# Kernel tuning notes

Measured on AMD Instinct MI355X. Metric: run time of the kernel, lower is better.

The kernel has to match this reference:

```python
import jax, jax.numpy as jnp
import numpy as np

N = 100000   # nodes
C = 128      # in_channels
K = 32       # n_super_nodes
B = 64       # graphs (num segments)


def setup_inputs() -> dict:
    key = jax.random.key(0)
    k_x, k_b, k_w1, k_b1, k_w2, k_b2 = jax.random.split(key, 6)
    x = jax.random.normal(k_x, (N, C), dtype=jnp.float32)
    batch = jnp.sort(jax.random.randint(k_b, (N,), 0, B))
    # assign_mlp params: Linear(C,C) -> ReLU -> Linear(C,K); stored as [in,out]
    W1 = jax.random.normal(k_w1, (C, C), dtype=jnp.float32) / np.sqrt(C)
    b1 = jax.random.normal(k_b1, (C,), dtype=jnp.float32) * 0.01
    W2 = jax.random.normal(k_w2, (C, K), dtype=jnp.float32) / np.sqrt(C)
    b2 = jax.random.normal(k_b2, (K,), dtype=jnp.float32) * 0.01
    return {"x": x, "batch": batch, "W1": W1, "b1": b1, "W2": W2, "b2": b2}


def reference(x, batch, W1, b1, W2, b2):
    # assignment logits: MLP over node features
    h = jax.nn.relu(x @ W1 + b1)          # [N, C]
    s = jax.nn.softmax(h @ W2 + b2, axis=-1)  # [N, K]
    # outer product per node, then scatter-sum by graph id
    x_expanded = x[:, None, :] * s[:, :, None]  # [N, K, C]
    out = jax.ops.segment_sum(x_expanded, batch, num_segments=B)  # [B, K, C]
    return (out, s)
```

## Files before the change

### kernel.cpp

```cpp
#include <hip/hip_runtime.h>
#include <hip/hip_bf16.h>

#define NN 100000
#define CC 128
#define KK 32
#define BB 64

typedef __bf16 bf16x8 __attribute__((ext_vector_type(8)));
typedef float  f32x4  __attribute__((ext_vector_type(4)));

__device__ __forceinline__ unsigned short f2bf(float v) {
    union { float f; unsigned u; } a; a.f = v;
    unsigned r = a.u + 0x7FFF + ((a.u >> 16) & 1);
    return (unsigned short)(r >> 16);
}
__device__ __forceinline__ float bf2f(unsigned short h) {
    union { unsigned u; float f; } a; a.u = ((unsigned)h) << 16;
    return a.f;
}

__global__ __launch_bounds__(256) void hp_prep(const int* __restrict__ batch,
                                               const float* __restrict__ W1,
                                               int* __restrict__ bounds,
                                               unsigned short* __restrict__ w1f) {
    const int t = blockIdx.x * 256 + threadIdx.x;
    if (blockIdx.x == 0 && threadIdx.x <= BB) {
        const int b = threadIdx.x;
        int lo = 0, hi = NN;
        while (lo < hi) {
            const int mid = (lo + hi) >> 1;
            if (batch[mid] < b) lo = mid + 1; else hi = mid;
        }
        bounds[b] = lo;
    }
    for (int idx = t; idx < 16384; idx += 2048) {
        const int j    = idx & 7;
        const int lane = (idx >> 3) & 63;
        const int nt   = (idx >> 9) & 7;
        const int kt   = idx >> 12;
        const int k = kt * 32 + (lane >> 4) * 8 + j;
        const int n = nt * 16 + (lane & 15);
        const float w = W1[k * CC + n];
        const unsigned short h = f2bf(w);
        w1f[idx]         = h;
        w1f[16384 + idx] = f2bf(w - bf2f(h));
    }
}

__global__ __launch_bounds__(256, 3) void hp_mlp(
    const float* __restrict__ x,
    const unsigned short* __restrict__ w1f,
    const float* __restrict__ b1,
    const float* __restrict__ W2,
    const float* __restrict__ b2,
    float* __restrict__ s_out)
{
    __shared__ __align__(16) char uni[33280];
    __shared__ float lgT[KK * 66];

    unsigned short* xa = (unsigned short*)uni;
    float*          hs = (float*)uni;

    const int t    = threadIdx.x;
    const int wave = __builtin_amdgcn_readfirstlane(t >> 6);
    const int lane = t & 63;
    const int base = blockIdx.x * 64;
    const int nvalid = min(64, NN - base);

    #pragma unroll
    for (int p = 0; p < 4; ++p) {
        const int q  = wave + 4 * p;
        const int mt = q >> 2, kt = q & 3;
        int n = base + mt * 16 + (lane & 15);
        if (n >= NN) n = NN - 1;
        const int ck = kt * 32 + (lane >> 4) * 8;
        const float4 va = *(const float4*)(x + (size_t)n * CC + ck);
        const float4 vb = *(const float4*)(x + (size_t)n * CC + ck + 4);
        float v[8] = {va.x, va.y, va.z, va.w, vb.x, vb.y, vb.z, vb.w};
        unsigned short hi[8], lo[8];
        #pragma unroll
        for (int j = 0; j < 8; ++j) {
            hi[j] = f2bf(v[j]);
            lo[j] = f2bf(v[j] - bf2f(hi[j]));
        }
        unsigned short* d0 = xa + (q * 64 + lane) * 8;
        unsigned short* d1 = d0 + 8192;
        *(ushort4*)(d0)     = make_ushort4(hi[0], hi[1], hi[2], hi[3]);
        *(ushort4*)(d0 + 4) = make_ushort4(hi[4], hi[5], hi[6], hi[7]);
        *(ushort4*)(d1)     = make_ushort4(lo[0], lo[1], lo[2], lo[3]);
        *(ushort4*)(d1 + 4) = make_ushort4(lo[4], lo[5], lo[6], lo[7]);
    }
    __syncthreads();

    f32x4 acc[4][2];
    #pragma unroll
    for (int mt = 0; mt < 4; ++mt)
        #pragma unroll
        for (int nl = 0; nl < 2; ++nl)
            acc[mt][nl] = (f32x4){0.f, 0.f, 0.f, 0.f};

    for (int kt = 0; kt < 4; ++kt) {
        bf16x8 ah[4], al[4];
        #pragma unroll
        for (int mt = 0; mt < 4; ++mt) {
            ah[mt] = *(const bf16x8*)(xa + ((mt * 4 + kt) * 64 + lane) * 8);
            al[mt] = *(const bf16x8*)(xa + 8192 + ((mt * 4 + kt) * 64 + lane) * 8);
        }
        #pragma unroll
        for (int nl = 0; nl < 2; ++nl) {
            const int nt = 2 * wave + nl;
            const bf16x8 wh = *(const bf16x8*)(w1f + ((kt * 8 + nt) * 64 + lane) * 8);
            const bf16x8 wl = *(const bf16x8*)(w1f + 16384 + ((kt * 8 + nt) * 64 + lane) * 8);
            #pragma unroll
            for (int mt = 0; mt < 4; ++mt) {
                acc[mt][nl] = __builtin_amdgcn_mfma_f32_16x16x32_bf16(ah[mt], wh, acc[mt][nl], 0, 0, 0);
                acc[mt][nl] = __builtin_amdgcn_mfma_f32_16x16x32_bf16(al[mt], wh, acc[mt][nl], 0, 0, 0);
                acc[mt][nl] = __builtin_amdgcn_mfma_f32_16x16x32_bf16(ah[mt], wl, acc[mt][nl], 0, 0, 0);
            }
        }
    }
    __syncthreads();

    {
        const int cA = 2 * wave * 16 + (lane & 15);
        const int cB = cA + 16;
        const float bvA = b1[cA], bvB = b1[cB];
        #pragma unroll
        for (int mt = 0; mt < 4; ++mt) {
            #pragma unroll
            for (int r = 0; r < 4; ++r) {
                const int node = mt * 16 + (lane >> 4) * 4 + r;
                hs[node * 130 + cA] = fmaxf(acc[mt][0][r] + bvA, 0.f);
                hs[node * 130 + cB] = fmaxf(acc[mt][1][r] + bvB, 0.f);
            }
        }
    }
    __syncthreads();

    {
        const int kw = 8 * wave;
        float lg[8];
        #pragma unroll
        for (int j = 0; j < 8; ++j) lg[j] = 0.f;
        const float* hrow = hs + lane * 130;
        #pragma unroll 4
        for (int c = 0; c < CC; c += 2) {
            const float2 hv = *(const float2*)(hrow + c);
            const float* Wr = W2 + c * KK + kw;
            #pragma unroll
            for (int j = 0; j < 8; ++j) lg[j] = fmaf(hv.x, Wr[j], lg[j]);
            #pragma unroll
            for (int j = 0; j < 8; ++j) lg[j] = fmaf(hv.y, Wr[KK + j], lg[j]);
        }
        #pragma unroll
        for (int j = 0; j < 8; ++j)
            lgT[(kw + j) * 66 + lane] = lg[j] + b2[kw + j];
    }
    __syncthreads();

    if (wave == 0) {
        float v[KK];
        float m = -3.4e38f;
        #pragma unroll
        for (int k = 0; k < KK; ++k) {
            v[k] = lgT[k * 66 + lane];
            m = fmaxf(m, v[k]);
        }
        float sum = 0.f;
        #pragma unroll
        for (int k = 0; k < KK; ++k) {
            v[k] = __expf(v[k] - m);
            sum += v[k];
        }
        const float inv = 1.f / sum;
        if (lane < nvalid) {
            float* gp = s_out + (size_t)(base + lane) * KK;
            #pragma unroll
            for (int k = 0; k < KK; k += 4)
                *(float4*)(gp + k) = make_float4(v[k] * inv, v[k+1] * inv,
                                                 v[k+2] * inv, v[k+3] * inv);
        }
    }
}

__global__ __launch_bounds__(256) void hp_pool(
    const float* __restrict__ x,
    const float* __restrict__ s,
    const int* __restrict__ bounds,
    float* __restrict__ part,
    int nslices)
{
    const int b = blockIdx.x / nslices;
    const int p = blockIdx.x - b * nslices;
    const int t = threadIdx.x;

    const int gs  = bounds[b];
    const int cnt = bounds[b + 1] - gs;
    const int n0  = gs + (int)(((long long)cnt * p) / nslices);
    const int n1  = gs + (int)(((long long)cnt * (p + 1)) / nslices);

    const int k0 = (t >> 5) * 4;
    const int c0 = (t & 31) * 4;

    float a4[4][4] = {{0.f}};

    #pragma unroll 2
    for (int n = n0; n < n1; ++n) {
        const float4 xv = *(const float4*)(x + (size_t)n * CC + c0);
        const float4 sv = *(const float4*)(s + (size_t)n * KK + k0);
        a4[0][0] = fmaf(sv.x, xv.x, a4[0][0]); a4[0][1] = fmaf(sv.x, xv.y, a4[0][1]);
        a4[0][2] = fmaf(sv.x, xv.z, a4[0][2]); a4[0][3] = fmaf(sv.x, xv.w, a4[0][3]);
        a4[1][0] = fmaf(sv.y, xv.x, a4[1][0]); a4[1][1] = fmaf(sv.y, xv.y, a4[1][1]);
        a4[1][2] = fmaf(sv.y, xv.z, a4[1][2]); a4[1][3] = fmaf(sv.y, xv.w, a4[1][3]);
        a4[2][0] = fmaf(sv.z, xv.x, a4[2][0]); a4[2][1] = fmaf(sv.z, xv.y, a4[2][1]);
        a4[2][2] = fmaf(sv.z, xv.z, a4[2][2]); a4[2][3] = fmaf(sv.z, xv.w, a4[2][3]);
        a4[3][0] = fmaf(sv.w, xv.x, a4[3][0]); a4[3][1] = fmaf(sv.w, xv.y, a4[3][1]);
        a4[3][2] = fmaf(sv.w, xv.z, a4[3][2]); a4[3][3] = fmaf(sv.w, xv.w, a4[3][3]);
    }

    float* op = part + (size_t)blockIdx.x * KK * CC;
    #pragma unroll
    for (int a = 0; a < 4; ++a)
        *(float4*)&op[(k0 + a) * CC + c0] = make_float4(a4[a][0], a4[a][1], a4[a][2], a4[a][3]);
}

__global__ __launch_bounds__(256) void hp_reduce(const float* __restrict__ part,
                                                 float* __restrict__ out,
                                                 int nslices) {
    const int i = (blockIdx.x * 256 + threadIdx.x) * 4;
    if (i < BB * KK * CC) {
        const int b = i >> 12;
        const int j = i & 4095;
        const float* pp = part + (size_t)b * nslices * 4096 + j;
        float4 r = make_float4(0.f, 0.f, 0.f, 0.f);
        for (int q = 0; q < nslices; ++q) {
            float4 v = *(const float4*)(pp + (size_t)q * 4096);
            r.x += v.x; r.y += v.y; r.z += v.z; r.w += v.w;
        }
        *(float4*)(out + i) = r;
    }
}

extern "C" void kernel_launch(void* const* d_in, const int* in_sizes, int n_in,
                              void* d_out, int out_size, void* d_ws, size_t ws_size,
                              hipStream_t stream) {
    const float* x     = (const float*)d_in[0];
    const int*   batch = (const int*)d_in[1];
    const float* W1    = (const float*)d_in[2];
    const float* b1    = (const float*)d_in[3];
    const float* W2    = (const float*)d_in[4];
    const float* b2    = (const float*)d_in[5];

    float* out = (float*)d_out;
    float* s   = out + (size_t)BB * KK * CC;

    int*            bounds = (int*)d_ws;
    unsigned short* w1f    = (unsigned short*)((char*)d_ws + 1024);
    float*          part   = (float*)((char*)d_ws + 1024 + 65536);

    int nslices = 16;
    while (nslices > 4 &&
           ws_size < 1024 + 65536 + (size_t)BB * nslices * KK * CC * 4)
        nslices >>= 1;

    hp_prep<<<8, 256, 0, stream>>>(batch, W1, bounds, w1f);
    hp_mlp<<<(NN + 63) / 64, 256, 0, stream>>>(x, w1f, b1, W2, b2, s);
    hp_pool<<<BB * nslices, 256, 0, stream>>>(x, s, bounds, part, nslices);
    hp_reduce<<<BB * KK * CC / (256 * 4), 256, 0, stream>>>(part, out, nslices);
}
```

Measured before the change: 164.6 us.

## Shrink MLP tiles, parallelize softmax across waves, fuse reduce into pool

The MLP kernel now handles 32 nodes per block instead of 64, with half the shared memory and a launch bound asking for 8 blocks per CU. The second layer and softmax are spread across all four waves, using shuffle and shared-memory max/sum reductions in place of a single wave doing the softmax. The separate reduce kernel is removed: the last pool block for each graph, detected with an atomic counter, sums the partials itself. The default slice count drops from 16 to 8. This saves a kernel launch and raises occupancy, at the cost of extra syncs and a serialized final reduction per graph.

```diff
diff --git a/kernel.cpp b/kernel.cpp
--- a/kernel.cpp
+++ b/kernel.cpp
@@ -22,17 +22,22 @@
 __global__ __launch_bounds__(256) void hp_prep(const int* __restrict__ batch,
                                                const float* __restrict__ W1,
                                                int* __restrict__ bounds,
+                                               int* __restrict__ counters,
                                                unsigned short* __restrict__ w1f) {
+    if (blockIdx.x == 0) {
+        if (threadIdx.x <= BB) {
+            const int b = threadIdx.x;
+            int lo = 0, hi = NN;
+            while (lo < hi) {
+                const int mid = (lo + hi) >> 1;
+                if (batch[mid] < b) lo = mid + 1; else hi = mid;
+            }
+            bounds[b] = lo;
+        }
+        if (threadIdx.x >= 128 && threadIdx.x < 128 + BB)
+            counters[threadIdx.x - 128] = 0;
+    }
     const int t = blockIdx.x * 256 + threadIdx.x;
-    if (blockIdx.x == 0 && threadIdx.x <= BB) {
-        const int b = threadIdx.x;
-        int lo = 0, hi = NN;
-        while (lo < hi) {
-            const int mid = (lo + hi) >> 1;
-            if (batch[mid] < b) lo = mid + 1; else hi = mid;
-        }
-        bounds[b] = lo;
-    }
     for (int idx = t; idx < 16384; idx += 2048) {
         const int j    = idx & 7;
         const int lane = (idx >> 3) & 63;
@@ -47,7 +52,7 @@
     }
 }
 
-__global__ __launch_bounds__(256, 3) void hp_mlp(
+__global__ __launch_bounds__(256, 8) void hp_mlp(
     const float* __restrict__ x,
     const unsigned short* __restrict__ w1f,
     const float* __restrict__ b1,
@@ -55,8 +60,9 @@
     const float* __restrict__ b2,
     float* __restrict__ s_out)
 {
-    __shared__ __align__(16) char uni[33280];
-    __shared__ float lgT[KK * 66];
+    __shared__ __align__(16) char uni[16640];
+    __shared__ float redm[4][32];
+    __shared__ float reds[4][32];
 
     unsigned short* xa = (unsigned short*)uni;
     float*          hs = (float*)uni;
@@ -64,19 +70,16 @@
     const int t    = threadIdx.x;
     const int wave = __builtin_amdgcn_readfirstlane(t >> 6);
     const int lane = t & 63;
-    const int base = blockIdx.x * 64;
-    const int nvalid = min(64, NN - base);
-
-    #pragma unroll
-    for (int p = 0; p < 4; ++p) {
-        const int q  = wave + 4 * p;
-        const int mt = q >> 2, kt = q & 3;
-        int n = base + mt * 16 + (lane & 15);
-        if (n >= NN) n = NN - 1;
-        const int ck = kt * 32 + (lane >> 4) * 8;
+    const int base = blockIdx.x * 32;
+
+    #pragma unroll
+    for (int mt = 0; mt < 2; ++mt) {
+        const int q  = mt * 4 + wave;
+        const int n  = base + mt * 16 + (lane & 15);
+        const int ck = wave * 32 + (lane >> 4) * 8;
         const float4 va = *(const float4*)(x + (size_t)n * CC + ck);
         const float4 vb = *(const float4*)(x + (size_t)n * CC + ck + 4);
-        float v[8] = {va.x, va.y, va.z, va.w, vb.x, vb.y, vb.z, vb.w};
+        const float v[8] = {va.x, va.y, va.z, va.w, vb.x, vb.y, vb.z, vb.w};
         unsigned short hi[8], lo[8];
         #pragma unroll
         for (int j = 0; j < 8; ++j) {
@@ -84,7 +87,7 @@
             lo[j] = f2bf(v[j] - bf2f(hi[j]));
         }
         unsigned short* d0 = xa + (q * 64 + lane) * 8;
-        unsigned short* d1 = d0 + 8192;
+        unsigned short* d1 = d0 + 4096;
         *(ushort4*)(d0)     = make_ushort4(hi[0], hi[1], hi[2], hi[3]);
         *(ushort4*)(d0 + 4) = make_ushort4(hi[4], hi[5], hi[6], hi[7]);
         *(ushort4*)(d1)     = make_ushort4(lo[0], lo[1], lo[2], lo[3]);
@@ -92,19 +95,20 @@
     }
     __syncthreads();
 
-    f32x4 acc[4][2];
-    #pragma unroll
-    for (int mt = 0; mt < 4; ++mt)
+    f32x4 acc[2][2];
+    #pragma unroll
+    for (int mt = 0; mt < 2; ++mt)
         #pragma unroll
         for (int nl = 0; nl < 2; ++nl)
             acc[mt][nl] = (f32x4){0.f, 0.f, 0.f, 0.f};
 
+    #pragma unroll
     for (int kt = 0; kt < 4; ++kt) {
-        bf16x8 ah[4], al[4];
-        #pragma unroll
-        for (int mt = 0; mt < 4; ++mt) {
+        bf16x8 ah[2], al[2];
+        #pragma unroll
+        for (int mt = 0; mt < 2; ++mt) {
             ah[mt] = *(const bf16x8*)(xa + ((mt * 4 + kt) * 64 + lane) * 8);
-            al[mt] = *(const bf16x8*)(xa + 8192 + ((mt * 4 + kt) * 64 + lane) * 8);
+            al[mt] = *(const bf16x8*)(xa + 4096 + ((mt * 4 + kt) * 64 + lane) * 8);
         }
         #pragma unroll
         for (int nl = 0; nl < 2; ++nl) {
@@ -112,7 +116,7 @@
             const bf16x8 wh = *(const bf16x8*)(w1f + ((kt * 8 + nt) * 64 + lane) * 8);
             const bf16x8 wl = *(const bf16x8*)(w1f + 16384 + ((kt * 8 + nt) * 64 + lane) * 8);
             #pragma unroll
-            for (int mt = 0; mt < 4; ++mt) {
+            for (int mt = 0; mt < 2; ++mt) {
                 acc[mt][nl] = __builtin_amdgcn_mfma_f32_16x16x32_bf16(ah[mt], wh, acc[mt][nl], 0, 0, 0);
                 acc[mt][nl] = __builtin_amdgcn_mfma_f32_16x16x32_bf16(al[mt], wh, acc[mt][nl], 0, 0, 0);
                 acc[mt][nl] = __builtin_amdgcn_mfma_f32_16x16x32_bf16(ah[mt], wl, acc[mt][nl], 0, 0, 0);
@@ -121,66 +125,54 @@
     }
     __syncthreads();
 
-    {
-        const int cA = 2 * wave * 16 + (lane & 15);
-        const int cB = cA + 16;
-        const float bvA = b1[cA], bvB = b1[cB];
-        #pragma unroll
-        for (int mt = 0; mt < 4; ++mt) {
+    #pragma unroll
+    for (int nl = 0; nl < 2; ++nl) {
+        const int c = (2 * wave + nl) * 16 + (lane & 15);
+        const float bv = b1[c];
+        #pragma unroll
+        for (int mt = 0; mt < 2; ++mt)
             #pragma unroll
             for (int r = 0; r < 4; ++r) {
                 const int node = mt * 16 + (lane >> 4) * 4 + r;
-                hs[node * 130 + cA] = fmaxf(acc[mt][0][r] + bvA, 0.f);
-                hs[node * 130 + cB] = fmaxf(acc[mt][1][r] + bvB, 0.f);
-            }
-        }
-    }
-    __syncthreads();
-
-    {
-        const int kw = 8 * wave;
-        float lg[8];
-        #pragma unroll
-        for (int j = 0; j < 8; ++j) lg[j] = 0.f;
-        const float* hrow = hs + lane * 130;
-        #pragma unroll 4
-        for (int c = 0; c < CC; c += 2) {
-            const float2 hv = *(const float2*)(hrow + c);
-            const float* Wr = W2 + c * KK + kw;
-            #pragma unroll
-            for (int j = 0; j < 8; ++j) lg[j] = fmaf(hv.x, Wr[j], lg[j]);
-            #pragma unroll
-            for (int j = 0; j < 8; ++j) lg[j] = fmaf(hv.y, Wr[KK + j], lg[j]);
-        }
-        #pragma unroll
-        for (int j = 0; j < 8; ++j)
-            lgT[(kw + j) * 66 + lane] = lg[j] + b2[kw + j];
-    }
-    __syncthreads();
-
-    if (wave == 0) {
-        float v[KK];
-        float m = -3.4e38f;
-        #pragma unroll
-        for (int k = 0; k < KK; ++k) {
-            v[k] = lgT[k * 66 + lane];
-            m = fmaxf(m, v[k]);
-        }
-        float sum = 0.f;
-        #pragma unroll
-        for (int k = 0; k < KK; ++k) {
-            v[k] = __expf(v[k] - m);
-            sum += v[k];
-        }
-        const float inv = 1.f / sum;
-        if (lane < nvalid) {
-            float* gp = s_out + (size_t)(base + lane) * KK;
-            #pragma unroll
-            for (int k = 0; k < KK; k += 4)
-                *(float4*)(gp + k) = make_float4(v[k] * inv, v[k+1] * inv,
-                                                 v[k+2] * inv, v[k+3] * inv);
-        }
-    }
+                hs[node * 130 + c] = fmaxf(acc[mt][nl][r] + bv, 0.f);
+            }
+    }
+    __syncthreads();
+
+    const int node = lane & 31;
+    const int koff = ((lane >> 5) << 4) + wave * 4;
+    float4 bv2 = *(const float4*)(b2 + koff);
+    float lg[4] = {bv2.x, bv2.y, bv2.z, bv2.w};
+    const float* hrow = hs + node * 130;
+    #pragma unroll 4
+    for (int c = 0; c < CC; c += 2) {
+        const float2 hv = *(const float2*)(hrow + c);
+        const float4 w0 = *(const float4*)(W2 + c * KK + koff);
+        const float4 w1 = *(const float4*)(W2 + (c + 1) * KK + koff);
+        lg[0] = fmaf(hv.x, w0.x, lg[0]); lg[1] = fmaf(hv.x, w0.y, lg[1]);
+        lg[2] = fmaf(hv.x, w0.z, lg[2]); lg[3] = fmaf(hv.x, w0.w, lg[3]);
+        lg[0] = fmaf(hv.y, w1.x, lg[0]); lg[1] = fmaf(hv.y, w1.y, lg[1]);
+        lg[2] = fmaf(hv.y, w1.z, lg[2]); lg[3] = fmaf(hv.y, w1.w, lg[3]);
+    }
+
+    float m = fmaxf(fmaxf(lg[0], lg[1]), fmaxf(lg[2], lg[3]));
+    m = fmaxf(m, __shfl_xor(m, 32));
+    if (lane < 32) redm[wave][lane] = m;
+    __syncthreads();
+    const float M = fmaxf(fmaxf(redm[0][node], redm[1][node]),
+                          fmaxf(redm[2][node], redm[3][node]));
+    const float e0 = __expf(lg[0] - M);
+    const float e1 = __expf(lg[1] - M);
+    const float e2 = __expf(lg[2] - M);
+    const float e3 = __expf(lg[3] - M);
+    float sp = (e0 + e1) + (e2 + e3);
+    sp += __shfl_xor(sp, 32);
+    if (lane < 32) reds[wave][lane] = sp;
+    __syncthreads();
+    const float S = (reds[0][node] + reds[1][node]) + (reds[2][node] + reds[3][node]);
+    const float inv = 1.f / S;
+    *(float4*)(s_out + (size_t)(base + node) * KK + koff) =
+        make_float4(e0 * inv, e1 * inv, e2 * inv, e3 * inv);
 }
 
 __global__ __launch_bounds__(256) void hp_pool(
@@ -188,8 +180,12 @@
     const float* __restrict__ s,
     const int* __restrict__ bounds,
     float* __restrict__ part,
+    int* __restrict__ counters,
+    float* __restrict__ out,
     int nslices)
 {
+    __shared__ int sflag;
+
     const int b = blockIdx.x / nslices;
     const int p = blockIdx.x - b * nslices;
     const int t = threadIdx.x;
@@ -204,7 +200,7 @@
 
     float a4[4][4] = {{0.f}};
 
-    #pragma unroll 2
+    #pragma unroll 4
     for (int n = n0; n < n1; ++n) {
         const float4 xv = *(const float4*)(x + (size_t)n * CC + c0);
         const float4 sv = *(const float4*)(s + (size_t)n * KK + k0);
@@ -221,23 +217,28 @@
     float* op = part + (size_t)blockIdx.x * KK * CC;
     #pragma unroll
     for (int a = 0; a < 4; ++a)
-        *(float4*)&op[(k0 + a) * CC + c0] = make_float4(a4[a][0], a4[a][1], a4[a][2], a4[a][3]);
-}
-
-__global__ __launch_bounds__(256) void hp_reduce(const float* __restrict__ part,
-                                                 float* __restrict__ out,
-                                                 int nslices) {
-    const int i = (blockIdx.x * 256 + threadIdx.x) * 4;
-    if (i < BB * KK * CC) {
-        const int b = i >> 12;
-        const int j = i & 4095;
-        const float* pp = part + (size_t)b * nslices * 4096 + j;
-        float4 r = make_float4(0.f, 0.f, 0.f, 0.f);
-        for (int q = 0; q < nslices; ++q) {
-            float4 v = *(const float4*)(pp + (size_t)q * 4096);
-            r.x += v.x; r.y += v.y; r.z += v.z; r.w += v.w;
-        }
-        *(float4*)(out + i) = r;
+        *(float4*)&op[(k0 + a) * CC + c0] =
+            make_float4(a4[a][0], a4[a][1], a4[a][2], a4[a][3]);
+
+    __threadfence();
+    if (t == 0) {
+        const int old = atomicAdd(counters + b, 1);
+        sflag = (old == nslices - 1);
+    }
+    __syncthreads();
+    if (sflag) {
+        __threadfence();
+        const float* pp = part + (size_t)b * nslices * KK * CC;
+        #pragma unroll
+        for (int a = 0; a < 4; ++a) {
+            const int j = (k0 + a) * CC + c0;
+            float4 r = make_float4(0.f, 0.f, 0.f, 0.f);
+            for (int q = 0; q < nslices; ++q) {
+                const float4 v = *(const float4*)(pp + (size_t)q * KK * CC + j);
+                r.x += v.x; r.y += v.y; r.z += v.z; r.w += v.w;
+            }
+            *(float4*)(out + (size_t)b * KK * CC + j) = r;
+        }
     }
 }
 
@@ -254,17 +255,16 @@
     float* out = (float*)d_out;
     float* s   = out + (size_t)BB * KK * CC;
 
-    int*            bounds = (int*)d_ws;
-    unsigned short* w1f    = (unsigned short*)((char*)d_ws + 1024);
-    float*          part   = (float*)((char*)d_ws + 1024 + 65536);
-
-    int nslices = 16;
-    while (nslices > 4 &&
-           ws_size < 1024 + 65536 + (size_t)BB * nslices * KK * CC * 4)
-        nslices >>= 1;
-
-    hp_prep<<<8, 256, 0, stream>>>(batch, W1, bounds, w1f);
-    hp_mlp<<<(NN + 63) / 64, 256, 0, stream>>>(x, w1f, b1, W2, b2, s);
-    hp_pool<<<BB * nslices, 256, 0, stream>>>(x, s, bounds, part, nslices);
-    hp_reduce<<<BB * KK * CC / (256 * 4), 256, 0, stream>>>(part, out, nslices);
-}
+    int*            bounds   = (int*)d_ws;
+    int*            counters = (int*)((char*)d_ws + 512);
+    unsigned short* w1f      = (unsigned short*)((char*)d_ws + 1024);
+    float*          part     = (float*)((char*)d_ws + 1024 + 65536);
+
+    int nslices = 8;
+    if (ws_size < 1024 + 65536 + (size_t)BB * 8 * KK * CC * 4)
+        nslices = 4;
+
+    hp_prep<<<8, 256, 0, stream>>>(batch, W1, bounds, counters, w1f);
+    hp_mlp<<<NN / 32, 256, 0, stream>>>(x, w1f, b1, W2, b2, s);
+    hp_pool<<<BB * nslices, 256, 0, stream>>>(x, s, bounds, part, counters, out, nslices);
+}
```

Measured after the change: 258.5 us. 57.0% more time.
